# Performance work log

Measured on AMD Instinct MI355X. Metric: run time of the kernel, lower is better.

The kernel has to match this reference:

```python
import jax, jax.numpy as jnp
import numpy as np

N, C = 50000, 256
H, D = 8, 64          # num_heads, out_channels (per-head dim)
M = 64                # nb_random_features
EPS = 1e-6


def _create_projection_matrix(m, d, seed=0):
    """Performer orthogonal random features: stacked orthogonal blocks scaled by chi-norms."""
    rng = np.random.RandomState(seed)
    blocks = []
    nb_full = m // d
    for _ in range(nb_full):
        q, _ = np.linalg.qr(rng.randn(d, d))
        blocks.append(q.T)
    rem = m - nb_full * d
    if rem > 0:
        q, _ = np.linalg.qr(rng.randn(d, d))
        blocks.append(q.T[:rem])
    multiplier = np.linalg.norm(rng.randn(m, d), axis=1)  # scaling == 0 path
    return (multiplier[:, None] * np.vstack(blocks)).astype(np.float32)


def setup_inputs() -> dict:
    key = jax.random.key(0)
    ks = jax.random.split(key, 9)
    s = 0.05  # small init so exp() of random features stays well-conditioned
    return {
        "x":     jax.random.normal(ks[0], (N, C), dtype=jnp.float32),
        "Wq_w":  jax.random.normal(ks[1], (C, H * D), dtype=jnp.float32) * s,
        "Wq_b":  jnp.zeros((H * D,), dtype=jnp.float32),
        "Wk_w":  jax.random.normal(ks[2], (C, H * D), dtype=jnp.float32) * s,
        "Wk_b":  jnp.zeros((H * D,), dtype=jnp.float32),
        "Wv_w":  jax.random.normal(ks[3], (C, H * D), dtype=jnp.float32) * s,
        "Wv_b":  jnp.zeros((H * D,), dtype=jnp.float32),
        "Wo_w":  jax.random.normal(ks[4], (H * D, D), dtype=jnp.float32) * s,
        "Wo_b":  jnp.zeros((D,), dtype=jnp.float32),
        "proj":  jnp.asarray(_create_projection_matrix(M, D, seed=0)),  # [M, D]
    }


def _softmax_kernel(data, proj):
    # data: [B,N,H,D], proj: [M,D]
    data_normalizer = 1.0 / jnp.sqrt(jnp.sqrt(jnp.float32(data.shape[-1])))
    ratio = 1.0 / jnp.sqrt(jnp.float32(proj.shape[0]))
    data_dash = ratio * jnp.einsum("bnhd,md->bnhm", data_normalizer * data, proj)
    return jnp.exp(data_dash) + EPS


def reference(x, Wq_w, Wq_b, Wk_w, Wk_b, Wv_w, Wv_b, Wo_w, Wo_b, proj):
    xb = x[None]  # [1, N, C]
    B, n, _ = xb.shape
    Q = (xb @ Wq_w + Wq_b).reshape(B, n, H, D)
    K = (xb @ Wk_w + Wk_b).reshape(B, n, H, D)
    V = (xb @ Wv_w + Wv_b).reshape(B, n, H, D)

    Qp = _softmax_kernel(Q, proj)  # [B,N,H,M]
    Kp = _softmax_kernel(K, proj)  # [B,N,H,M]

    KV = jnp.einsum("bnhm,bnhd->bhmd", Kp, V)          # [B,H,M,D]
    Z_num = jnp.einsum("bnhm,bhmd->bnhd", Qp, KV)      # [B,N,H,D]
    Kp_sum = jnp.sum(Kp, axis=1)                        # [B,H,M]
    Z_den = jnp.einsum("bnhm,bhm->bnh", Qp, Kp_sum)[..., None]
    Z = (Z_num / (Z_den + EPS)).reshape(B, n, H * D)
    out = Z @ Wo_w + Wo_b                               # [B,N,D]
    return out[0]                                       # squeeze batch -> [N,D]
```

## Files before the change

kernel.cpp:

```cpp
#include <hip/hip_runtime.h>


#define NN      50000
#define HDIM    512
#define EPSF    1e-6f
#define SCALE   0.044194173824159224f
#define NCHK    196
#define KSLICE  28
#define NOUT    391
#define WP      264
#define TP      72
#define LDPB    36

typedef __bf16 bf16;
typedef __bf16 bf16x4 __attribute__((ext_vector_type(4)));
typedef __bf16 bf16x8 __attribute__((ext_vector_type(8)));
typedef float  f32x4  __attribute__((ext_vector_type(4)));

#define MFMA(a, b, c) __builtin_amdgcn_mfma_f32_16x16x32_bf16((a), (b), (c), 0, 0, 0)

__device__ __forceinline__ void lds_fence() {
    asm volatile("s_waitcnt lgkmcnt(0)" ::: "memory");
}

__global__ void prepx_kernel(const float* __restrict__ x, bf16* __restrict__ xb,
                             const float* __restrict__ Wq, const float* __restrict__ bq,
                             const float* __restrict__ Wk, const float* __restrict__ bk,
                             const float* __restrict__ Wv, const float* __restrict__ Wo,
                             const float* __restrict__ proj,
                             bf16* __restrict__ WqpT, bf16* __restrict__ WkpT,
                             bf16* __restrict__ WvT, bf16* __restrict__ WoT,
                             float* __restrict__ fqb, float* __restrict__ fkb)
{
    if (blockIdx.x < 2048) {
        for (int i8 = blockIdx.x * 256 + threadIdx.x; i8 < NN * 256 / 8;
             i8 += 2048 * 256) {
            const float4 a = reinterpret_cast<const float4*>(x)[i8 * 2];
            const float4 b = reinterpret_cast<const float4*>(x)[i8 * 2 + 1];
            bf16x8 r;
            r[0] = (bf16)a.x; r[1] = (bf16)a.y; r[2] = (bf16)a.z; r[3] = (bf16)a.w;
            r[4] = (bf16)b.x; r[5] = (bf16)b.y; r[6] = (bf16)b.z; r[7] = (bf16)b.w;
            reinterpret_cast<bf16x8*>(xb)[i8] = r;
        }
        return;
    }
    const int t = (blockIdx.x - 2048) * 256 + threadIdx.x;
    if (t < 131072) {
        const int row = t >> 8, c = t & 255;
        const int hh = row >> 6, m = row & 63;
        const float* pr = proj + m * 64;
        const float* wq = Wq + (size_t)c * HDIM + hh * 64;
        const float* wk = Wk + (size_t)c * HDIM + hh * 64;
        float sq = 0.f, sk = 0.f;
        for (int d = 0; d < 64; ++d) { const float p = pr[d]; sq += wq[d] * p; sk += wk[d] * p; }
        WqpT[(size_t)row * 256 + c] = (bf16)sq;
        WkpT[(size_t)row * 256 + c] = (bf16)sk;
    } else if (t < 262144) {
        const int i = t - 131072;
        const int col = i >> 8, c = i & 255;
        WvT[i] = (bf16)Wv[(size_t)c * HDIM + col];
    } else if (t < 262144 + 32768) {
        const int i = t - 262144;
        const int j = i >> 9, dp = i & 511;
        WoT[i] = (bf16)Wo[(size_t)dp * 64 + j];
    } else if (t < 262144 + 32768 + 1024) {
        const int i = t - 262144 - 32768;
        const int which = i >> 9, row = i & 511;
        const int hh = row >> 6, m = row & 63;
        const float* pr = proj + m * 64;
        const float* b = (which ? bk : bq) + hh * 64;
        float s = 0.f;
        for (int d = 0; d < 64; ++d) s += b[d] * pr[d];
        (which ? fkb : fqb)[row] = s;
    }
}

__global__ __launch_bounds__(512)
void kv_kernel(const bf16* __restrict__ xb,
               const bf16* __restrict__ WkpT, const float* __restrict__ fkb,
               const bf16* __restrict__ WvT,  const float* __restrict__ bv,
               float* __restrict__ pKV, float* __restrict__ pSum)
{
    __shared__ __align__(16) bf16 wk_lds[64 * WP];
    __shared__ __align__(16) bf16 wv_lds[64 * WP];
    __shared__ __align__(16) bf16 bufs[8][2][64 * LDPB];

    const int t     = threadIdx.x;
    const int w     = t >> 6;
    const int l     = t & 63;
    const int lr    = l & 15;
    const int lk    = l >> 4;
    const int slice = blockIdx.x;
    const int hd    = blockIdx.y;

    for (int i = t; i < 2048; i += 512) {
        const int row = i >> 5, c8 = i & 31;
        *reinterpret_cast<bf16x8*>(&wk_lds[row * WP + c8 * 8]) =
            *reinterpret_cast<const bf16x8*>(&WkpT[(size_t)(hd * 64 + row) * 256 + c8 * 8]);
        *reinterpret_cast<bf16x8*>(&wv_lds[row * WP + c8 * 8]) =
            *reinterpret_cast<const bf16x8*>(&WvT[(size_t)(hd * 64 + row) * 256 + c8 * 8]);
    }

    bf16* kptbuf = bufs[w][0];
    bf16* vtbuf  = bufs[w][1];

    f32x4 kvacc[16];
#pragma unroll
    for (int i = 0; i < 16; ++i) kvacc[i] = (f32x4){0.f, 0.f, 0.f, 0.f};
    float ksum_acc[4] = {0.f, 0.f, 0.f, 0.f};

    float fkbc[4], bvc[4];
#pragma unroll
    for (int q = 0; q < 4; ++q) {
        fkbc[q] = fkb[hd * 64 + q * 16 + lr];
        bvc [q] = bv [hd * 64 + q * 16 + lr];
    }
    __syncthreads();

    for (int chunk = slice; chunk < NCHK; chunk += KSLICE) {
        const int nbase = chunk * 256 + w * 32;

#pragma unroll
        for (int rt = 0; rt < 2; ++rt) {
            const bf16* xr = xb + (size_t)min(nbase + rt * 16 + lr, NN - 1) * 256;
            bf16x8 xa[8];
#pragma unroll
            for (int kk = 0; kk < 8; ++kk)
                xa[kk] = *reinterpret_cast<const bf16x8*>(xr + kk * 32 + lk * 8);

            f32x4 fK[4];
#pragma unroll
            for (int q = 0; q < 4; ++q)
                fK[q] = (f32x4){fkbc[q], fkbc[q], fkbc[q], fkbc[q]};
#pragma unroll
            for (int kk = 0; kk < 8; ++kk) {
                const int off = kk * 32 + lk * 8;
#pragma unroll
                for (int mt = 0; mt < 4; ++mt) {
                    const bf16x8 wb = *reinterpret_cast<const bf16x8*>(
                        &wk_lds[(mt * 16 + lr) * WP + off]);
                    fK[mt] = MFMA(xa[kk], wb, fK[mt]);
                }
            }
            if (rt == 0)
                lds_fence();
#pragma unroll
            for (int q = 0; q < 4; ++q) {
                bf16x4 kp4;
#pragma unroll
                for (int r = 0; r < 4; ++r) {
                    const int nl = rt * 16 + lk * 4 + r;
                    const float kpv = ((nbase + nl) < NN)
                                          ? (__expf(SCALE * fK[q][r]) + EPSF) : 0.f;
                    ksum_acc[q] += kpv;
                    kp4[r] = (bf16)kpv;
                }
                *reinterpret_cast<bf16x4*>(
                    &kptbuf[(q * 16 + lr) * LDPB + rt * 16 + lk * 4]) = kp4;
            }

            f32x4 aV[4];
#pragma unroll
            for (int q = 0; q < 4; ++q)
                aV[q] = (f32x4){bvc[q], bvc[q], bvc[q], bvc[q]};
#pragma unroll
            for (int kk = 0; kk < 8; ++kk) {
                const int off = kk * 32 + lk * 8;
#pragma unroll
                for (int dt = 0; dt < 4; ++dt) {
                    const bf16x8 wb = *reinterpret_cast<const bf16x8*>(
                        &wv_lds[(dt * 16 + lr) * WP + off]);
                    aV[dt] = MFMA(xa[kk], wb, aV[dt]);
                }
            }
#pragma unroll
            for (int q = 0; q < 4; ++q) {
                bf16x4 vv4;
#pragma unroll
                for (int r = 0; r < 4; ++r) {
                    const int nl = rt * 16 + lk * 4 + r;
                    vv4[r] = ((nbase + nl) < NN) ? (bf16)aV[q][r] : (bf16)0.f;
                }
                *reinterpret_cast<bf16x4*>(
                    &vtbuf[(q * 16 + lr) * LDPB + rt * 16 + lk * 4]) = vv4;
            }
        }
        lds_fence();

        bf16x8 kpa[4], vb[4];
#pragma unroll
        for (int mt = 0; mt < 4; ++mt)
            kpa[mt] = *reinterpret_cast<const bf16x8*>(
                &kptbuf[(mt * 16 + lr) * LDPB + lk * 8]);
#pragma unroll
        for (int dt = 0; dt < 4; ++dt)
            vb[dt] = *reinterpret_cast<const bf16x8*>(
                &vtbuf[(dt * 16 + lr) * LDPB + lk * 8]);
#pragma unroll
        for (int mt = 0; mt < 4; ++mt)
#pragma unroll
            for (int dt = 0; dt < 4; ++dt)
                kvacc[mt * 4 + dt] = MFMA(kpa[mt], vb[dt], kvacc[mt * 4 + dt]);
    }

#pragma unroll
    for (int q = 0; q < 4; ++q) {
        float s = ksum_acc[q];
        s += __shfl_xor(s, 16, 64);
        s += __shfl_xor(s, 32, 64);
        ksum_acc[q] = s;
    }
    float* red  = (float*)(&bufs[0][0][0]);
    float* reds = red + 4096;

    __syncthreads();
    for (int i = 0; i < 8; ++i) {
        if (w == i) {
#pragma unroll
            for (int mt = 0; mt < 4; ++mt)
#pragma unroll
                for (int dt = 0; dt < 4; ++dt)
#pragma unroll
                    for (int r = 0; r < 4; ++r) {
                        const int md = (mt * 16 + lk * 4 + r) * 64 + dt * 16 + lr;
                        if (i == 0) red[md] = kvacc[mt * 4 + dt][r];
                        else        red[md] += kvacc[mt * 4 + dt][r];
                    }
            if (lk == 0) {
#pragma unroll
                for (int q = 0; q < 4; ++q) {
                    if (i == 0) reds[q * 16 + lr] = ksum_acc[q];
                    else        reds[q * 16 + lr] += ksum_acc[q];
                }
            }
        }
        __syncthreads();
    }
    float* dst = pKV + ((size_t)hd * KSLICE + slice) * 4096;
    for (int i = t; i < 4096; i += 512) dst[i] = red[i];
    if (t < 64) pSum[((size_t)hd * KSLICE + slice) * 64 + t] = reds[t];
}

__global__ void reduce_kernel(const float* __restrict__ pKV, const float* __restrict__ pSum,
                              bf16* __restrict__ KVT, float* __restrict__ Ksum)
{
    const int idx = blockIdx.x * 256 + threadIdx.x;
    if (idx < 8 * 4096) {
        const int h = idx >> 12, md = idx & 4095;
        const int m = md >> 6, d = md & 63;
        float s = 0.f;
        for (int b = 0; b < KSLICE; ++b) s += pKV[((size_t)h * KSLICE + b) * 4096 + md];
        KVT[h * 4096 + d * 64 + m] = (bf16)s;
    } else if (idx < 8 * 4096 + 512) {
        const int j = idx - 8 * 4096;
        const int h = j >> 6, m = j & 63;
        float s = 0.f;
        for (int b = 0; b < KSLICE; ++b) s += pSum[((size_t)h * KSLICE + b) * 64 + m];
        Ksum[j] = s;
    }
}

__global__ __launch_bounds__(512)
void out_kernel(const bf16* __restrict__ xb,
                const bf16* __restrict__ WqpT, const float* __restrict__ fqb,
                const bf16* __restrict__ KVT, const float* __restrict__ Ksum,
                const bf16* __restrict__ WoT, const float* __restrict__ bo,
                float* __restrict__ out)
{
    __shared__ __align__(16) bf16 wq_lds[64 * WP];
    __shared__ __align__(16) bf16 kvt_lds[64 * TP];
    __shared__ __align__(16) bf16 wo_lds[64 * TP];
    __shared__ __align__(16) bf16 tbufs[8][16 * TP];

    const int t  = threadIdx.x;
    const int w  = t >> 6;
    const int l  = t & 63;
    const int lr = l & 15;
    const int lk = l >> 4;
    bf16* tbuf = tbufs[w];
    const int nbase = blockIdx.x * 128 + w * 16;

    const bf16* xr = xb + (size_t)min(nbase + lr, NN - 1) * 256;
    bf16x8 xa[8];
#pragma unroll
    for (int kk = 0; kk < 8; ++kk)
        xa[kk] = *reinterpret_cast<const bf16x8*>(xr + kk * 32 + lk * 8);

    f32x4 oacc[4];
#pragma unroll
    for (int jt = 0; jt < 4; ++jt) {
        const float b = bo[jt * 16 + lr];
        oacc[jt] = (f32x4){b, b, b, b};
    }

    for (int h = 0; h < 8; ++h) {
        __syncthreads();
        for (int i = t; i < 2048; i += 512) {
            const int row = i >> 5, c8 = i & 31;
            *reinterpret_cast<bf16x8*>(&wq_lds[row * WP + c8 * 8]) =
                *reinterpret_cast<const bf16x8*>(&WqpT[(size_t)(h * 64 + row) * 256 + c8 * 8]);
        }
        {
            const int row = t >> 3, c8 = t & 7;
            *reinterpret_cast<bf16x8*>(&kvt_lds[row * TP + c8 * 8]) =
                *reinterpret_cast<const bf16x8*>(&KVT[h * 4096 + row * 64 + c8 * 8]);
            *reinterpret_cast<bf16x8*>(&wo_lds[row * TP + c8 * 8]) =
                *reinterpret_cast<const bf16x8*>(&WoT[(size_t)row * HDIM + h * 64 + c8 * 8]);
        }
        __syncthreads();

        f32x4 fQ[4];
#pragma unroll
        for (int mt = 0; mt < 4; ++mt) {
            const float b = fqb[h * 64 + mt * 16 + lr];
            fQ[mt] = (f32x4){b, b, b, b};
        }
#pragma unroll
        for (int kk = 0; kk < 8; ++kk) {
            const int off = kk * 32 + lk * 8;
#pragma unroll
            for (int mt = 0; mt < 4; ++mt) {
                const bf16x8 wb = *reinterpret_cast<const bf16x8*>(
                    &wq_lds[(mt * 16 + lr) * WP + off]);
                fQ[mt] = MFMA(xa[kk], wb, fQ[mt]);
            }
        }

        lds_fence();
        float denp[4] = {0.f, 0.f, 0.f, 0.f};
#pragma unroll
        for (int mt = 0; mt < 4; ++mt) {
            const float ks = Ksum[h * 64 + mt * 16 + lr];
#pragma unroll
            for (int r = 0; r < 4; ++r) {
                const float qp = __expf(SCALE * fQ[mt][r]) + EPSF;
                denp[r] += qp * ks;
                tbuf[(lk * 4 + r) * TP + mt * 16 + lr] = (bf16)qp;
            }
        }
#pragma unroll
        for (int r = 0; r < 4; ++r) {
            float s = denp[r];
            s += __shfl_xor(s, 1, 64);
            s += __shfl_xor(s, 2, 64);
            s += __shfl_xor(s, 4, 64);
            s += __shfl_xor(s, 8, 64);
            denp[r] = s;
        }
        lds_fence();

        bf16x8 qpa[2];
#pragma unroll
        for (int kk = 0; kk < 2; ++kk)
            qpa[kk] = *reinterpret_cast<const bf16x8*>(
                &tbuf[lr * TP + kk * 32 + lk * 8]);
        f32x4 num[4];
#pragma unroll
        for (int dt = 0; dt < 4; ++dt) num[dt] = (f32x4){0.f, 0.f, 0.f, 0.f};
#pragma unroll
        for (int dt = 0; dt < 4; ++dt)
#pragma unroll
            for (int kk = 0; kk < 2; ++kk) {
                const bf16x8 kvb = *reinterpret_cast<const bf16x8*>(
                    &kvt_lds[(dt * 16 + lr) * TP + kk * 32 + lk * 8]);
                num[dt] = MFMA(qpa[kk], kvb, num[dt]);
            }

        lds_fence();
#pragma unroll
        for (int dt = 0; dt < 4; ++dt)
#pragma unroll
            for (int r = 0; r < 4; ++r)
                tbuf[(lk * 4 + r) * TP + dt * 16 + lr] =
                    (bf16)(num[dt][r] / (denp[r] + EPSF));
        lds_fence();

        bf16x8 za[2];
#pragma unroll
        for (int kk = 0; kk < 2; ++kk)
            za[kk] = *reinterpret_cast<const bf16x8*>(
                &tbuf[lr * TP + kk * 32 + lk * 8]);
#pragma unroll
        for (int jt = 0; jt < 4; ++jt)
#pragma unroll
            for (int kk = 0; kk < 2; ++kk) {
                const bf16x8 wo = *reinterpret_cast<const bf16x8*>(
                    &wo_lds[(jt * 16 + lr) * TP + kk * 32 + lk * 8]);
                oacc[jt] = MFMA(za[kk], wo, oacc[jt]);
            }
    }

#pragma unroll
    for (int jt = 0; jt < 4; ++jt)
#pragma unroll
        for (int r = 0; r < 4; ++r) {
            const int n = nbase + lk * 4 + r;
            if (n < NN) out[(size_t)n * 64 + jt * 16 + lr] = oacc[jt][r];
        }
}

extern "C" void kernel_launch(void* const* d_in, const int* in_sizes, int n_in,
                              void* d_out, int out_size, void* d_ws, size_t ws_size,
                              hipStream_t stream) {
    const float* x    = (const float*)d_in[0];
    const float* Wq   = (const float*)d_in[1];
    const float* bq   = (const float*)d_in[2];
    const float* Wk   = (const float*)d_in[3];
    const float* bk   = (const float*)d_in[4];
    const float* Wv   = (const float*)d_in[5];
    const float* bv   = (const float*)d_in[6];
    const float* Wo   = (const float*)d_in[7];
    const float* bo   = (const float*)d_in[8];
    const float* proj = (const float*)d_in[9];
    float* out = (float*)d_out;

    char* ws = (char*)d_ws;
    float* Ksum = (float*)(ws + 0);
    float* fqb  = (float*)(ws + 2048);
    float* fkb  = (float*)(ws + 4096);
    bf16*  WqpT = (bf16*)(ws + 6144);
    bf16*  WkpT = (bf16*)(ws + 268288);
    bf16*  WvT  = (bf16*)(ws + 530432);
    bf16*  WoT  = (bf16*)(ws + 792576);
    bf16*  KVT  = (bf16*)(ws + 858112);
    bf16*  xb   = (bf16*)(ws + 923648);
    float* pKV  = (float*)(ws + 26523648);
    float* pSum = (float*)(ws + 30193664);

    prepx_kernel<<<dim3(2048 + 1156), 256, 0, stream>>>(
        x, xb, Wq, bq, Wk, bk, Wv, Wo, proj, WqpT, WkpT, WvT, WoT, fqb, fkb);
    kv_kernel<<<dim3(KSLICE, 8), 512, 0, stream>>>(xb, WkpT, fkb, WvT, bv, pKV, pSum);
    reduce_kernel<<<dim3(130), 256, 0, stream>>>(pKV, pSum, KVT, Ksum);
    out_kernel<<<dim3(NOUT), 512, 0, stream>>>(xb, WqpT, fqb, KVT, Ksum,
                                               WoT, bo, out);
}
```

Measured before the change: 149.6 us.

## Process two 16-row tiles per wave in out_kernel to halve weight staging

Each wave in out_kernel now handles 32 rows (two 16-row sub-tiles) instead of 16, so a block covers 256 rows and the grid shrinks from 391 to 196 blocks. The per-head loads of Wq', KV^T and Wo into LDS, along with the syncthreads, are amortized over twice as many rows, and the KV and Wo fragments read from LDS are reused across both sub-tiles. The x rows are no longer held in registers across heads; they are reloaded from global memory (likely served from cache) on every head iteration to keep register pressure in check. The trade-offs are fewer blocks on the device, which may leave CUs underused, and extra global reloads of x.

```diff
diff --git a/kernel.cpp b/kernel.cpp
--- a/kernel.cpp
+++ b/kernel.cpp
@@ -7,7 +7,7 @@
 #define SCALE   0.044194173824159224f
 #define NCHK    196
 #define KSLICE  28
-#define NOUT    391
+#define NOUT    196
 #define WP      264
 #define TP      72
 #define LDPB    36
@@ -270,7 +270,7 @@
     __shared__ __align__(16) bf16 wq_lds[64 * WP];
     __shared__ __align__(16) bf16 kvt_lds[64 * TP];
     __shared__ __align__(16) bf16 wo_lds[64 * TP];
-    __shared__ __align__(16) bf16 tbufs[8][16 * TP];
+    __shared__ __align__(16) bf16 tbufs[8][32 * TP];
 
     const int t  = threadIdx.x;
     const int w  = t >> 6;
@@ -278,19 +278,17 @@
     const int lr = l & 15;
     const int lk = l >> 4;
     bf16* tbuf = tbufs[w];
-    const int nbase = blockIdx.x * 128 + w * 16;
-
-    const bf16* xr = xb + (size_t)min(nbase + lr, NN - 1) * 256;
-    bf16x8 xa[8];
-#pragma unroll
-    for (int kk = 0; kk < 8; ++kk)
-        xa[kk] = *reinterpret_cast<const bf16x8*>(xr + kk * 32 + lk * 8);
-
-    f32x4 oacc[4];
+    const int nbase = blockIdx.x * 256 + w * 32;
+
+    const bf16* xr0 = xb + (size_t)min(nbase + lr,      NN - 1) * 256;
+    const bf16* xr1 = xb + (size_t)min(nbase + 16 + lr, NN - 1) * 256;
+
+    f32x4 oacc[2][4];
 #pragma unroll
     for (int jt = 0; jt < 4; ++jt) {
         const float b = bo[jt * 16 + lr];
-        oacc[jt] = (f32x4){b, b, b, b};
+        oacc[0][jt] = (f32x4){b, b, b, b};
+        oacc[1][jt] = oacc[0][jt];
     }
 
     for (int h = 0; h < 8; ++h) {
@@ -309,94 +307,116 @@
         }
         __syncthreads();
 
-        f32x4 fQ[4];
-#pragma unroll
-        for (int mt = 0; mt < 4; ++mt) {
-            const float b = fqb[h * 64 + mt * 16 + lr];
-            fQ[mt] = (f32x4){b, b, b, b};
-        }
-#pragma unroll
-        for (int kk = 0; kk < 8; ++kk) {
-            const int off = kk * 32 + lk * 8;
+        float denp[2][4];
+#pragma unroll
+        for (int rt = 0; rt < 2; ++rt) {
+            const bf16* xr = rt ? xr1 : xr0;
+            bf16x8 xa[8];
+#pragma unroll
+            for (int kk = 0; kk < 8; ++kk)
+                xa[kk] = *reinterpret_cast<const bf16x8*>(xr + kk * 32 + lk * 8);
+
+            f32x4 fQ[4];
 #pragma unroll
             for (int mt = 0; mt < 4; ++mt) {
-                const bf16x8 wb = *reinterpret_cast<const bf16x8*>(
-                    &wq_lds[(mt * 16 + lr) * WP + off]);
-                fQ[mt] = MFMA(xa[kk], wb, fQ[mt]);
-            }
-        }
-
+                const float b = fqb[h * 64 + mt * 16 + lr];
+                fQ[mt] = (f32x4){b, b, b, b};
+            }
+#pragma unroll
+            for (int kk = 0; kk < 8; ++kk) {
+                const int off = kk * 32 + lk * 8;
+#pragma unroll
+                for (int mt = 0; mt < 4; ++mt) {
+                    const bf16x8 wb = *reinterpret_cast<const bf16x8*>(
+                        &wq_lds[(mt * 16 + lr) * WP + off]);
+                    fQ[mt] = MFMA(xa[kk], wb, fQ[mt]);
+                }
+            }
+
+            float dp[4] = {0.f, 0.f, 0.f, 0.f};
+#pragma unroll
+            for (int mt = 0; mt < 4; ++mt) {
+                const float ks = Ksum[h * 64 + mt * 16 + lr];
+#pragma unroll
+                for (int r = 0; r < 4; ++r) {
+                    const float qp = __expf(SCALE * fQ[mt][r]) + EPSF;
+                    dp[r] += qp * ks;
+                    tbuf[(rt * 16 + lk * 4 + r) * TP + mt * 16 + lr] = (bf16)qp;
+                }
+            }
+#pragma unroll
+            for (int r = 0; r < 4; ++r) {
+                float s = dp[r];
+                s += __shfl_xor(s, 1, 64);
+                s += __shfl_xor(s, 2, 64);
+                s += __shfl_xor(s, 4, 64);
+                s += __shfl_xor(s, 8, 64);
+                denp[rt][r] = s;
+            }
+        }
         lds_fence();
-        float denp[4] = {0.f, 0.f, 0.f, 0.f};
-#pragma unroll
-        for (int mt = 0; mt < 4; ++mt) {
-            const float ks = Ksum[h * 64 + mt * 16 + lr];
-#pragma unroll
-            for (int r = 0; r < 4; ++r) {
-                const float qp = __expf(SCALE * fQ[mt][r]) + EPSF;
-                denp[r] += qp * ks;
-                tbuf[(lk * 4 + r) * TP + mt * 16 + lr] = (bf16)qp;
-            }
-        }
-#pragma unroll
-        for (int r = 0; r < 4; ++r) {
-            float s = denp[r];
-            s += __shfl_xor(s, 1, 64);
-            s += __shfl_xor(s, 2, 64);
-            s += __shfl_xor(s, 4, 64);
-            s += __shfl_xor(s, 8, 64);
-            denp[r] = s;
-        }
-        lds_fence();
-
-        bf16x8 qpa[2];
-#pragma unroll
-        for (int kk = 0; kk < 2; ++kk)
-            qpa[kk] = *reinterpret_cast<const bf16x8*>(
-                &tbuf[lr * TP + kk * 32 + lk * 8]);
-        f32x4 num[4];
-#pragma unroll
-        for (int dt = 0; dt < 4; ++dt) num[dt] = (f32x4){0.f, 0.f, 0.f, 0.f};
+
+        bf16x8 qpa[2][2];
+#pragma unroll
+        for (int rt = 0; rt < 2; ++rt)
+#pragma unroll
+            for (int kk = 0; kk < 2; ++kk)
+                qpa[rt][kk] = *reinterpret_cast<const bf16x8*>(
+                    &tbuf[(rt * 16 + lr) * TP + kk * 32 + lk * 8]);
+        f32x4 num[2][4];
+#pragma unroll
+        for (int dt = 0; dt < 4; ++dt) {
+            num[0][dt] = (f32x4){0.f, 0.f, 0.f, 0.f};
+            num[1][dt] = num[0][dt];
+        }
 #pragma unroll
         for (int dt = 0; dt < 4; ++dt)
 #pragma unroll
             for (int kk = 0; kk < 2; ++kk) {
                 const bf16x8 kvb = *reinterpret_cast<const bf16x8*>(
                     &kvt_lds[(dt * 16 + lr) * TP + kk * 32 + lk * 8]);
-                num[dt] = MFMA(qpa[kk], kvb, num[dt]);
+                num[0][dt] = MFMA(qpa[0][kk], kvb, num[0][dt]);
+                num[1][dt] = MFMA(qpa[1][kk], kvb, num[1][dt]);
             }
 
         lds_fence();
 #pragma unroll
-        for (int dt = 0; dt < 4; ++dt)
-#pragma unroll
-            for (int r = 0; r < 4; ++r)
-                tbuf[(lk * 4 + r) * TP + dt * 16 + lr] =
-                    (bf16)(num[dt][r] / (denp[r] + EPSF));
+        for (int rt = 0; rt < 2; ++rt)
+#pragma unroll
+            for (int dt = 0; dt < 4; ++dt)
+#pragma unroll
+                for (int r = 0; r < 4; ++r)
+                    tbuf[(rt * 16 + lk * 4 + r) * TP + dt * 16 + lr] =
+                        (bf16)(num[rt][dt][r] / (denp[rt][r] + EPSF));
         lds_fence();
 
-        bf16x8 za[2];
-#pragma unroll
-        for (int kk = 0; kk < 2; ++kk)
-            za[kk] = *reinterpret_cast<const bf16x8*>(
-                &tbuf[lr * TP + kk * 32 + lk * 8]);
+        bf16x8 za[2][2];
+#pragma unroll
+        for (int rt = 0; rt < 2; ++rt)
+#pragma unroll
+            for (int kk = 0; kk < 2; ++kk)
+                za[rt][kk] = *reinterpret_cast<const bf16x8*>(
+                    &tbuf[(rt * 16 + lr) * TP + kk * 32 + lk * 8]);
 #pragma unroll
         for (int jt = 0; jt < 4; ++jt)
 #pragma unroll
             for (int kk = 0; kk < 2; ++kk) {
                 const bf16x8 wo = *reinterpret_cast<const bf16x8*>(
                     &wo_lds[(jt * 16 + lr) * TP + kk * 32 + lk * 8]);
-                oacc[jt] = MFMA(za[kk], wo, oacc[jt]);
-            }
-    }
-
-#pragma unroll
-    for (int jt = 0; jt < 4; ++jt)
-#pragma unroll
-        for (int r = 0; r < 4; ++r) {
-            const int n = nbase + lk * 4 + r;
-            if (n < NN) out[(size_t)n * 64 + jt * 16 + lr] = oacc[jt][r];
-        }
+                oacc[0][jt] = MFMA(za[0][kk], wo, oacc[0][jt]);
+                oacc[1][jt] = MFMA(za[1][kk], wo, oacc[1][jt]);
+            }
+    }
+
+#pragma unroll
+    for (int rt = 0; rt < 2; ++rt)
+#pragma unroll
+        for (int jt = 0; jt < 4; ++jt)
+#pragma unroll
+            for (int r = 0; r < 4; ++r) {
+                const int n = nbase + rt * 16 + lk * 4 + r;
+                if (n < NN) out[(size_t)n * 64 + jt * 16 + lr] = oacc[rt][jt][r];
+            }
 }
 
 extern "C" void kernel_launch(void* const* d_in, const int* in_sizes, int n_in,
```

New measurement: 157.2 us. 5.0% more time.
